# Performance work log

Hardware: AMD Instinct MI355X
Metric: run time of the kernel (lower is better)

## Reference

```python
import jax, jax.numpy as jnp
import numpy as np

N_NODES = 200000   # total graph nodes (var + constraint)
N_VAR   = 112000   # nodes with x[:,0]==1, placed first for static slicing
N_EDGES = 3200000  # avg degree 16
HID     = 64
BATCH   = 64       # fc output width == batch_size in the torch module
TW      = 8        # target_width; TW*(TW-1)=56; N_VAR = seq_len*56 with seq_len=2000


def setup_inputs() -> dict:
    key = jax.random.key(0)
    ks = jax.random.split(key, 8)
    x = jax.random.normal(ks[0], (N_NODES, 2), jnp.float32)
    # var_mask = (x[:,0] == 1): make the first N_VAR nodes variable nodes.
    x = x.at[:, 0].set(jnp.where(jnp.arange(N_NODES) < N_VAR, 1.0, 0.0))
    edge_index = jax.random.randint(ks[1], (2, N_EDGES), 0, N_NODES, jnp.int32)
    W1 = jax.random.normal(ks[2], (2, HID), jnp.float32) / np.sqrt(2.0)
    b1 = jnp.zeros((HID,), jnp.float32)
    W2 = jax.random.normal(ks[3], (HID, HID), jnp.float32) / np.sqrt(HID)
    b2 = jnp.zeros((HID,), jnp.float32)
    Wfc = jax.random.normal(ks[4], (HID, BATCH), jnp.float32) / np.sqrt(HID)
    bfc = jnp.zeros((BATCH,), jnp.float32)
    return {"x": x, "edge_index": edge_index, "W1": W1, "b1": b1,
            "W2": W2, "b2": b2, "Wfc": Wfc, "bfc": bfc}


def gcn_conv(x, src, dst, W, b):
    """PyG GCNConv: transform, then sym-normalized aggregation with self-loops."""
    h = x @ W                                   # [N, F_out]
    ones = jnp.ones(src.shape[0], x.dtype)
    deg = jax.ops.segment_sum(ones, dst, num_segments=N_NODES) + 1.0  # +1: self-loop
    dinv = jax.lax.rsqrt(deg)                   # deg >= 1, always safe
    norm = dinv[src] * dinv[dst]                # [E]
    agg = jax.ops.segment_sum(h[src] * norm[:, None], dst, num_segments=N_NODES)
    agg = agg + h * (dinv * dinv)[:, None]      # self-loop message, norm = dinv_i^2
    return agg + b


def reference(x, edge_index, W1, b1, W2, b2, Wfc, bfc):
    src, dst = edge_index[0], edge_index[1]
    h = jax.nn.relu(gcn_conv(x, src, dst, W1, b1))
    h = gcn_conv(h, src, dst, W2, b2)
    # var_mask == first N_VAR rows by construction (static slice for jit)
    out = jax.nn.relu(h[:N_VAR] @ Wfc + bfc)    # [N_VAR, BATCH]
    width = TW * (TW - 1)                       # 56
    seq_len = N_VAR // width                    # 2000
    return jnp.round(out.reshape(seq_len, BATCH, width))
```

## Files before the change

### kernel.cpp

```cpp
#include <hip/hip_runtime.h>
#include <math.h>

#define N_NODES 200000
#define N_VAR   112000
#define N_EDGES 3200000
#define CAP     64

#define NFINE    512
#define PSZ_F    391
#define FCAP     7168
#define BIN_CHUNK 8192
#define NB_BIN   391
#define NB_L1    12500

typedef int v4i __attribute__((ext_vector_type(4)));

__global__ void __launch_bounds__(512) k_bin(const int* __restrict__ src,
                                             const int* __restrict__ dst,
                                             int* __restrict__ bins,
                                             int* __restrict__ bcnt,
                                             const float* __restrict__ W2,
                                             const float* __restrict__ b2,
                                             const float* __restrict__ Wfc,
                                             const float* __restrict__ bfc,
                                             float* __restrict__ Wc,
                                             float* __restrict__ bc) {
    __shared__ int hist[NFINE];
    __shared__ int seg[NFINE];
    __shared__ int gb[NFINE];
    __shared__ int cur[NFINE];
    __shared__ int wsum[8];
    __shared__ int stg[BIN_CHUNK];
    __shared__ unsigned short stgb[BIN_CHUNK];
    int tid = threadIdx.x;
    int lane = tid & 63, wid = tid >> 6;
    hist[tid] = 0;
    __syncthreads();

    int base = blockIdx.x * BIN_CHUNK;
    int pk[4][4];
    int bk[4][4];
    bool val[4];
    #pragma unroll
    for (int i = 0; i < 4; ++i) {
        int e4 = base + (i * 512 + tid) * 4;
        val[i] = (e4 < N_EDGES);
        if (val[i]) {
            v4i d = __builtin_nontemporal_load((const v4i*)(dst + e4));
            v4i s = __builtin_nontemporal_load((const v4i*)(src + e4));
            int dd[4] = {d.x, d.y, d.z, d.w};
            int ss[4] = {s.x, s.y, s.z, s.w};
            #pragma unroll
            for (int q = 0; q < 4; ++q) {
                int bb2 = dd[q] / PSZ_F;
                int dl = dd[q] - bb2 * PSZ_F;
                pk[i][q] = (dl << 18) | ss[q];
                bk[i][q] = bb2;
                atomicAdd(&hist[bb2], 1);
            }
        }
    }
    __syncthreads();

    int h = hist[tid];
    int inc = h;
    #pragma unroll
    for (int d = 1; d < 64; d <<= 1) {
        int t = __shfl_up(inc, d);
        if (lane >= d) inc += t;
    }
    if (lane == 63) wsum[wid] = inc;
    __syncthreads();
    int pre = 0, tot = 0;
    #pragma unroll
    for (int k = 0; k < 8; ++k) {
        int s = wsum[k];
        pre += (k < wid) ? s : 0;
        tot += s;
    }
    int ex = pre + inc - h;
    seg[tid] = ex;
    cur[tid] = ex;
    gb[tid]  = atomicAdd(&bcnt[tid], h);
    __syncthreads();

    #pragma unroll
    for (int i = 0; i < 4; ++i) {
        if (val[i]) {
            #pragma unroll
            for (int q = 0; q < 4; ++q) {
                int p = atomicAdd(&cur[bk[i][q]], 1);
                stg[p]  = pk[i][q];
                stgb[p] = (unsigned short)bk[i][q];
            }
        }
    }
    __syncthreads();

    for (int i = tid; i < tot; i += 512) {
        int bb2 = stgb[i];
        int pos = gb[bb2] + (i - seg[bb2]);
        if (pos < FCAP)
            bins[(size_t)bb2 * FCAP + pos] = stg[i];
    }

    int b = blockIdx.x;
    if (b < 8) {
        int e = b * 512 + tid;
        int j = e >> 6, l2 = e & 63;
        double acc = 0.0;
        for (int m = 0; m < 64; ++m)
            acc += (double)W2[j * 64 + m] * (double)Wfc[m * 64 + l2];
        Wc[e] = (float)acc;
    } else if (b == 8 && tid < 64) {
        double acc = (double)bfc[tid];
        for (int m = 0; m < 64; ++m)
            acc += (double)b2[m] * (double)Wfc[m * 64 + tid];
        bc[tid] = (float)acc;
    }
}

__global__ void __launch_bounds__(512) k_sort(const int* __restrict__ bins,
                                              const int* __restrict__ bcnt,
                                              const float2* __restrict__ x2,
                                              int* __restrict__ cnt,
                                              float4* __restrict__ xdc,
                                              int* __restrict__ buf) {
    __shared__ int hist[NFINE];
    __shared__ int off[NFINE];
    __shared__ int cur[NFINE];
    __shared__ int wsum[8];
    __shared__ int sorted[FCAP];
    __shared__ unsigned short rowid[FCAP];
    int tid = threadIdx.x;
    int lane = tid & 63, wid = tid >> 6;
    int b = blockIdx.x;
    int n = bcnt[b];
    if (n > FCAP) n = FCAP;
    const int* __restrict__ bp = bins + (size_t)b * FCAP;

    hist[tid] = 0;
    __syncthreads();
    for (int i = tid; i < n; i += 512)
        atomicAdd(&hist[bp[i] >> 18], 1);
    __syncthreads();

    int h = hist[tid];

    int vg = b * PSZ_F + tid;
    if (tid < PSZ_F && vg < N_NODES) {
        cnt[vg] = h;
        float dvv = rsqrtf((float)h + 1.0f);
        float2 xv = x2[vg];
        xdc[vg] = make_float4(xv.x * dvv, xv.y * dvv, dvv, 0.0f);
    }

    int inc = h;
    #pragma unroll
    for (int d = 1; d < 64; d <<= 1) {
        int t = __shfl_up(inc, d);
        if (lane >= d) inc += t;
    }
    if (lane == 63) wsum[wid] = inc;
    __syncthreads();
    int pre = 0;
    #pragma unroll
    for (int k = 0; k < 8; ++k) {
        int s = wsum[k];
        pre += (k < wid) ? s : 0;
    }
    int ex = pre + inc - h;
    off[tid] = ex;
    cur[tid] = ex;
    __syncthreads();

    for (int i = tid; i < n; i += 512) {
        int pkv = bp[i];
        int dl = pkv >> 18;
        int p = atomicAdd(&cur[dl], 1);
        sorted[p] = pkv & 0x3FFFF;
        rowid[p]  = (unsigned short)dl;
    }
    __syncthreads();

    for (int i = tid; i < n; i += 512) {
        int dl = rowid[i];
        int slot = i - off[dl];
        if (slot < CAP)
            buf[(size_t)(b * PSZ_F + dl) * CAP + slot] = sorted[i];
    }
}

__global__ void __launch_bounds__(256, 4) k_l1a(const int* __restrict__ cnt,
                                                const int* __restrict__ buf,
                                                const float4* __restrict__ xdc,
                                                float4* __restrict__ zn) {
    __shared__ __align__(16) float2 pb2[4][64];
    int w = threadIdx.x >> 6, l = threadIdx.x & 63;
    float2* __restrict__ pbw = &pb2[w][0];
    int v0 = blockIdx.x * 16 + w;
    int cc0 = __builtin_amdgcn_readfirstlane(cnt[v0]);
    int cc1 = __builtin_amdgcn_readfirstlane(cnt[v0 + 4]);
    int cc2 = __builtin_amdgcn_readfirstlane(cnt[v0 + 8]);
    int cc3 = __builtin_amdgcn_readfirstlane(cnt[v0 + 12]);

    int nn[4];
    float2 g[4];
    float4 zs[4];
    #pragma unroll
    for (int it = 0; it < 4; ++it) {
        int v = v0 + it * 4;
        int c = (it == 0) ? cc0 : (it == 1) ? cc1 : (it == 2) ? cc2 : cc3;
        int n = (c < CAP) ? c : CAP;
        nn[it] = n;
        int ridx = __builtin_nontemporal_load(buf + v * CAP + l);
        int idx  = (l < n) ? ridx : v;
        g[it]  = *(const float2*)&xdc[idx];
        zs[it] = xdc[v];
    }

    #pragma unroll
    for (int it = 0; it < 4; ++it) {
        int v = v0 + it * 4;
        int n = nn[it];
        float4 self = zs[it];
        float dv = self.z;
        pbw[l] = g[it];

        float ax = self.x, ay = self.y;
        float bx = 0.0f,   by = 0.0f;
        int j = 0;
        for (; j + 16 <= n; j += 16) {
            float4 q0 = *(const float4*)&pbw[j +  0];
            float4 q1 = *(const float4*)&pbw[j +  2];
            float4 q2 = *(const float4*)&pbw[j +  4];
            float4 q3 = *(const float4*)&pbw[j +  6];
            float4 q4 = *(const float4*)&pbw[j +  8];
            float4 q5 = *(const float4*)&pbw[j + 10];
            float4 q6 = *(const float4*)&pbw[j + 12];
            float4 q7 = *(const float4*)&pbw[j + 14];
            ax += q0.x; ay += q0.y;  bx += q0.z; by += q0.w;
            ax += q1.x; ay += q1.y;  bx += q1.z; by += q1.w;
            ax += q2.x; ay += q2.y;  bx += q2.z; by += q2.w;
            ax += q3.x; ay += q3.y;  bx += q3.z; by += q3.w;
            ax += q4.x; ay += q4.y;  bx += q4.z; by += q4.w;
            ax += q5.x; ay += q5.y;  bx += q5.z; by += q5.w;
            ax += q6.x; ay += q6.y;  bx += q6.z; by += q6.w;
            ax += q7.x; ay += q7.y;  bx += q7.z; by += q7.w;
        }
        for (; j + 8 <= n; j += 8) {
            float4 q0 = *(const float4*)&pbw[j + 0];
            float4 q1 = *(const float4*)&pbw[j + 2];
            float4 q2 = *(const float4*)&pbw[j + 4];
            float4 q3 = *(const float4*)&pbw[j + 6];
            ax += q0.x; ay += q0.y;  bx += q0.z; by += q0.w;
            ax += q1.x; ay += q1.y;  bx += q1.z; by += q1.w;
            ax += q2.x; ay += q2.y;  bx += q2.z; by += q2.w;
            ax += q3.x; ay += q3.y;  bx += q3.z; by += q3.w;
        }
        for (; j < n; ++j) {
            float2 q = pbw[j];
            ax += q.x; ay += q.y;
        }
        if (l == 0)
            zn[v] = make_float4((ax + bx) * dv, (ay + by) * dv, dv, 0.0f);
    }
}

__global__ void __launch_bounds__(256, 4) k_l2(const int* __restrict__ cnt,
                                               const int* __restrict__ buf,
                                               const float4* __restrict__ zn,
                                               const float* __restrict__ W1,
                                               const float* __restrict__ b1,
                                               const float* __restrict__ Wc,
                                               const float* __restrict__ bc,
                                               float* __restrict__ out) {
    __shared__ __align__(16) float4 pb[4][64];
    __shared__ __align__(16) float  avs[4][64];
    int w = threadIdx.x >> 6, l = threadIdx.x & 63;
    float4* __restrict__ pbw = &pb[w][0];
    float*  __restrict__ avw = &avs[w][0];
    float wc[64];
    #pragma unroll
    for (int jv = 0; jv < 64; ++jv)
        wc[jv] = Wc[jv * 64 + l];
    float w1a = W1[l], w1b = W1[64 + l], bb = b1[l];
    float bcl = bc[l];
    int v0 = blockIdx.x * 16 + w;
    int cc0 = __builtin_amdgcn_readfirstlane(cnt[v0]);
    int cc1 = __builtin_amdgcn_readfirstlane(cnt[v0 + 4]);
    int cc2 = __builtin_amdgcn_readfirstlane(cnt[v0 + 8]);
    int cc3 = __builtin_amdgcn_readfirstlane(cnt[v0 + 12]);

    int nn[4];
    float4 p[4], zs[4];
    #pragma unroll
    for (int it = 0; it < 4; ++it) {
        int v = v0 + it * 4;
        int c = (it == 0) ? cc0 : (it == 1) ? cc1 : (it == 2) ? cc2 : cc3;
        int n = (c < CAP) ? c : CAP;
        nn[it] = n;
        int ridx = __builtin_nontemporal_load(buf + v * CAP + l);
        int idx  = (l < n) ? ridx : v;
        p[it]  = zn[idx];
        zs[it] = zn[v];
    }

    #pragma unroll
    for (int it = 0; it < 4; ++it) {
        int v = v0 + it * 4;
        int c = (it == 0) ? cc0 : (it == 1) ? cc1 : (it == 2) ? cc2 : cc3;
        int n = nn[it];
        float dv = rsqrtf((float)c + 1.0f);
        float4 zss = zs[it];

        pbw[l] = p[it];

        float acc0 = fmaxf(fmaf(zss.x, w1a, fmaf(zss.y, w1b, bb)), 0.0f) * zss.z;
        float acc1 = 0.0f;
        int j = 0;
        for (; j + 8 <= n; j += 8) {
            float4 q0 = pbw[j+0], q1 = pbw[j+1], q2 = pbw[j+2], q3 = pbw[j+3];
            float4 q4 = pbw[j+4], q5 = pbw[j+5], q6 = pbw[j+6], q7 = pbw[j+7];
            float h0 = fmaxf(fmaf(q0.x, w1a, fmaf(q0.y, w1b, bb)), 0.0f) * q0.z;
            float h1 = fmaxf(fmaf(q1.x, w1a, fmaf(q1.y, w1b, bb)), 0.0f) * q1.z;
            float h2 = fmaxf(fmaf(q2.x, w1a, fmaf(q2.y, w1b, bb)), 0.0f) * q2.z;
            float h3 = fmaxf(fmaf(q3.x, w1a, fmaf(q3.y, w1b, bb)), 0.0f) * q3.z;
            float h4 = fmaxf(fmaf(q4.x, w1a, fmaf(q4.y, w1b, bb)), 0.0f) * q4.z;
            float h5 = fmaxf(fmaf(q5.x, w1a, fmaf(q5.y, w1b, bb)), 0.0f) * q5.z;
            float h6 = fmaxf(fmaf(q6.x, w1a, fmaf(q6.y, w1b, bb)), 0.0f) * q6.z;
            float h7 = fmaxf(fmaf(q7.x, w1a, fmaf(q7.y, w1b, bb)), 0.0f) * q7.z;
            acc0 += (h0 + h1) + (h2 + h3);
            acc1 += (h4 + h5) + (h6 + h7);
        }
        for (; j + 4 <= n; j += 4) {
            float4 q0 = pbw[j+0], q1 = pbw[j+1], q2 = pbw[j+2], q3 = pbw[j+3];
            float h0 = fmaxf(fmaf(q0.x, w1a, fmaf(q0.y, w1b, bb)), 0.0f) * q0.z;
            float h1 = fmaxf(fmaf(q1.x, w1a, fmaf(q1.y, w1b, bb)), 0.0f) * q1.z;
            float h2 = fmaxf(fmaf(q2.x, w1a, fmaf(q2.y, w1b, bb)), 0.0f) * q2.z;
            float h3 = fmaxf(fmaf(q3.x, w1a, fmaf(q3.y, w1b, bb)), 0.0f) * q3.z;
            acc0 += (h0 + h1) + (h2 + h3);
        }
        for (; j < n; ++j) {
            float4 q0 = pbw[j];
            acc1 += fmaxf(fmaf(q0.x, w1a, fmaf(q0.y, w1b, bb)), 0.0f) * q0.z;
        }
        float Av = (acc0 + acc1) * dv;

        avw[l] = Av;

        float t0 = 0.0f, t1 = 0.0f, t2 = 0.0f, t3 = 0.0f;
        #pragma unroll
        for (int jj = 0; jj < 64; jj += 4) {
            float4 a4 = *(const float4*)&avw[jj];
            t0 = fmaf(a4.x, wc[jj + 0], t0);
            t1 = fmaf(a4.y, wc[jj + 1], t1);
            t2 = fmaf(a4.z, wc[jj + 2], t2);
            t3 = fmaf(a4.w, wc[jj + 3], t3);
        }
        float t = ((t0 + t1) + (t2 + t3)) + bcl;
        __builtin_nontemporal_store(rintf(fmaxf(t, 0.0f)), out + v * 64 + l);
    }
}


extern "C" void kernel_launch(void* const* d_in, const int* in_sizes, int n_in,
                              void* d_out, int out_size, void* d_ws, size_t ws_size,
                              hipStream_t stream) {
    const float* x    = (const float*)d_in[0];
    const int*   ei   = (const int*)  d_in[1];
    const float* W1   = (const float*)d_in[2];
    const float* b1   = (const float*)d_in[3];
    const float* W2   = (const float*)d_in[4];
    const float* b2   = (const float*)d_in[5];
    const float* Wfc  = (const float*)d_in[6];
    const float* bfc  = (const float*)d_in[7];
    float* out = (float*)d_out;

    const int* src = ei;
    const int* dst = ei + N_EDGES;

    char* ws = (char*)d_ws;
    int*    cnt    = (int*)   (ws + 0);
    float4* xdc    = (float4*)(ws + 800000);
    int*    bins   = (int*)   (ws + 4000000);
    int*    bcnt   = (int*)   (ws + 18680064);
    float4* zn     = (float4*)(ws + 15204096);
    int*    buf    = (int*)   (ws + 19204096);
    float*  Wc     = (float*) (ws + 70404096);
    float*  bc     = (float*) (ws + 70420480);

    hipMemsetAsync(bcnt, 0, NFINE * sizeof(int), stream);
    k_bin  <<<NB_BIN, 512, 0, stream>>>(src, dst, bins, bcnt, W2, b2, Wfc, bfc, Wc, bc);
    k_sort <<<NFINE, 512, 0, stream>>>(bins, bcnt, (const float2*)x, cnt, xdc, buf);
    k_l1a  <<<NB_L1, 256, 0, stream>>>(cnt, buf, xdc, zn);
    k_l2   <<<N_VAR / 16, 256, 0, stream>>>(cnt, buf, zn, W1, b1, Wc, bc, out);
}
```

Baseline: 198.8 us.

## Switch neighbor lists from padded fixed-cap rows to compact CSR layout

The sort kernel now computes a global exclusive prefix over bin counts and writes neighbor indices contiguously (CSR-style) instead of into 64-slot padded rows per node. The row offset and the degree, clamped to 127, are packed into one int per node. The aggregation kernels decode offset and count and read only valid entries. This shrinks the adjacency buffer and its write and read traffic. The costs are a redundant per-block prefix scan in k_sort and a degree clamp at 127 that could change results for very high-degree nodes.

```diff
diff --git a/kernel.cpp b/kernel.cpp
--- a/kernel.cpp
+++ b/kernel.cpp
@@ -123,37 +123,46 @@
 __global__ void __launch_bounds__(512) k_sort(const int* __restrict__ bins,
                                               const int* __restrict__ bcnt,
                                               const float2* __restrict__ x2,
-                                              int* __restrict__ cnt,
+                                              int* __restrict__ cnt2,
                                               float4* __restrict__ xdc,
-                                              int* __restrict__ buf) {
+                                              int* __restrict__ buf2) {
     __shared__ int hist[NFINE];
     __shared__ int off[NFINE];
     __shared__ int cur[NFINE];
     __shared__ int wsum[8];
-    __shared__ int sorted[FCAP];
-    __shared__ unsigned short rowid[FCAP];
+    __shared__ int ebs;
+    __shared__ int sorted_pk[FCAP];
     int tid = threadIdx.x;
     int lane = tid & 63, wid = tid >> 6;
     int b = blockIdx.x;
-    int n = bcnt[b];
-    if (n > FCAP) n = FCAP;
+
+    int ec = bcnt[tid];
+    if (ec > FCAP) ec = FCAP;
+    int incE = ec;
+    #pragma unroll
+    for (int d = 1; d < 64; d <<= 1) {
+        int t = __shfl_up(incE, d);
+        if (lane >= d) incE += t;
+    }
+    if (lane == 63) wsum[wid] = incE;
+    __syncthreads();
+    int preE = 0;
+    #pragma unroll
+    for (int k = 0; k < 8; ++k)
+        preE += (k < wid) ? wsum[k] : 0;
+    if (tid == b) ebs = preE + incE - ec;
+    hist[tid] = 0;
+    __syncthreads();
+    int ebase = ebs;
+    int nb = bcnt[b];
+    if (nb > FCAP) nb = FCAP;
     const int* __restrict__ bp = bins + (size_t)b * FCAP;
 
-    hist[tid] = 0;
-    __syncthreads();
-    for (int i = tid; i < n; i += 512)
+    for (int i = tid; i < nb; i += 512)
         atomicAdd(&hist[bp[i] >> 18], 1);
     __syncthreads();
 
     int h = hist[tid];
-
-    int vg = b * PSZ_F + tid;
-    if (tid < PSZ_F && vg < N_NODES) {
-        cnt[vg] = h;
-        float dvv = rsqrtf((float)h + 1.0f);
-        float2 xv = x2[vg];
-        xdc[vg] = make_float4(xv.x * dvv, xv.y * dvv, dvv, 0.0f);
-    }
 
     int inc = h;
     #pragma unroll
@@ -165,44 +174,45 @@
     __syncthreads();
     int pre = 0;
     #pragma unroll
-    for (int k = 0; k < 8; ++k) {
-        int s = wsum[k];
-        pre += (k < wid) ? s : 0;
-    }
+    for (int k = 0; k < 8; ++k)
+        pre += (k < wid) ? wsum[k] : 0;
     int ex = pre + inc - h;
     off[tid] = ex;
     cur[tid] = ex;
-    __syncthreads();
-
-    for (int i = tid; i < n; i += 512) {
+
+    int vg = b * PSZ_F + tid;
+    if (tid < PSZ_F && vg < N_NODES) {
+        int ct = (h < 127) ? h : 127;
+        cnt2[vg] = ((ebase + ex) << 7) | ct;
+        float dvv = rsqrtf((float)ct + 1.0f);
+        float2 xv = x2[vg];
+        xdc[vg] = make_float4(xv.x * dvv, xv.y * dvv, dvv, 0.0f);
+    }
+    __syncthreads();
+
+    for (int i = tid; i < nb; i += 512) {
         int pkv = bp[i];
-        int dl = pkv >> 18;
-        int p = atomicAdd(&cur[dl], 1);
-        sorted[p] = pkv & 0x3FFFF;
-        rowid[p]  = (unsigned short)dl;
-    }
-    __syncthreads();
-
-    for (int i = tid; i < n; i += 512) {
-        int dl = rowid[i];
-        int slot = i - off[dl];
-        if (slot < CAP)
-            buf[(size_t)(b * PSZ_F + dl) * CAP + slot] = sorted[i];
-    }
+        int p = atomicAdd(&cur[pkv >> 18], 1);
+        sorted_pk[p] = pkv;
+    }
+    __syncthreads();
+
+    for (int i = tid; i < nb; i += 512)
+        buf2[ebase + i] = sorted_pk[i] & 0x3FFFF;
 }
 
-__global__ void __launch_bounds__(256, 4) k_l1a(const int* __restrict__ cnt,
-                                                const int* __restrict__ buf,
+__global__ void __launch_bounds__(256, 4) k_l1a(const int* __restrict__ cnt2,
+                                                const int* __restrict__ buf2,
                                                 const float4* __restrict__ xdc,
                                                 float4* __restrict__ zn) {
     __shared__ __align__(16) float2 pb2[4][64];
     int w = threadIdx.x >> 6, l = threadIdx.x & 63;
     float2* __restrict__ pbw = &pb2[w][0];
     int v0 = blockIdx.x * 16 + w;
-    int cc0 = __builtin_amdgcn_readfirstlane(cnt[v0]);
-    int cc1 = __builtin_amdgcn_readfirstlane(cnt[v0 + 4]);
-    int cc2 = __builtin_amdgcn_readfirstlane(cnt[v0 + 8]);
-    int cc3 = __builtin_amdgcn_readfirstlane(cnt[v0 + 12]);
+    int q0 = __builtin_amdgcn_readfirstlane(cnt2[v0]);
+    int q1 = __builtin_amdgcn_readfirstlane(cnt2[v0 + 4]);
+    int q2 = __builtin_amdgcn_readfirstlane(cnt2[v0 + 8]);
+    int q3 = __builtin_amdgcn_readfirstlane(cnt2[v0 + 12]);
 
     int nn[4];
     float2 g[4];
@@ -210,12 +220,14 @@
     #pragma unroll
     for (int it = 0; it < 4; ++it) {
         int v = v0 + it * 4;
-        int c = (it == 0) ? cc0 : (it == 1) ? cc1 : (it == 2) ? cc2 : cc3;
+        int q = (it == 0) ? q0 : (it == 1) ? q1 : (it == 2) ? q2 : q3;
+        int c = q & 127;
         int n = (c < CAP) ? c : CAP;
+        int rp = ((unsigned)q) >> 7;
         nn[it] = n;
-        int ridx = __builtin_nontemporal_load(buf + v * CAP + l);
-        int idx  = (l < n) ? ridx : v;
-        g[it]  = *(const float2*)&xdc[idx];
+        int ridx = v;
+        if (l < n) ridx = __builtin_nontemporal_load(buf2 + rp + l);
+        g[it]  = *(const float2*)&xdc[ridx];
         zs[it] = xdc[v];
     }
 
@@ -231,44 +243,44 @@
         float bx = 0.0f,   by = 0.0f;
         int j = 0;
         for (; j + 16 <= n; j += 16) {
-            float4 q0 = *(const float4*)&pbw[j +  0];
-            float4 q1 = *(const float4*)&pbw[j +  2];
-            float4 q2 = *(const float4*)&pbw[j +  4];
-            float4 q3 = *(const float4*)&pbw[j +  6];
-            float4 q4 = *(const float4*)&pbw[j +  8];
-            float4 q5 = *(const float4*)&pbw[j + 10];
-            float4 q6 = *(const float4*)&pbw[j + 12];
-            float4 q7 = *(const float4*)&pbw[j + 14];
-            ax += q0.x; ay += q0.y;  bx += q0.z; by += q0.w;
-            ax += q1.x; ay += q1.y;  bx += q1.z; by += q1.w;
-            ax += q2.x; ay += q2.y;  bx += q2.z; by += q2.w;
-            ax += q3.x; ay += q3.y;  bx += q3.z; by += q3.w;
-            ax += q4.x; ay += q4.y;  bx += q4.z; by += q4.w;
-            ax += q5.x; ay += q5.y;  bx += q5.z; by += q5.w;
-            ax += q6.x; ay += q6.y;  bx += q6.z; by += q6.w;
-            ax += q7.x; ay += q7.y;  bx += q7.z; by += q7.w;
+            float4 t0 = *(const float4*)&pbw[j +  0];
+            float4 t1 = *(const float4*)&pbw[j +  2];
+            float4 t2 = *(const float4*)&pbw[j +  4];
+            float4 t3 = *(const float4*)&pbw[j +  6];
+            float4 t4 = *(const float4*)&pbw[j +  8];
+            float4 t5 = *(const float4*)&pbw[j + 10];
+            float4 t6 = *(const float4*)&pbw[j + 12];
+            float4 t7 = *(const float4*)&pbw[j + 14];
+            ax += t0.x; ay += t0.y;  bx += t0.z; by += t0.w;
+            ax += t1.x; ay += t1.y;  bx += t1.z; by += t1.w;
+            ax += t2.x; ay += t2.y;  bx += t2.z; by += t2.w;
+            ax += t3.x; ay += t3.y;  bx += t3.z; by += t3.w;
+            ax += t4.x; ay += t4.y;  bx += t4.z; by += t4.w;
+            ax += t5.x; ay += t5.y;  bx += t5.z; by += t5.w;
+            ax += t6.x; ay += t6.y;  bx += t6.z; by += t6.w;
+            ax += t7.x; ay += t7.y;  bx += t7.z; by += t7.w;
         }
         for (; j + 8 <= n; j += 8) {
-            float4 q0 = *(const float4*)&pbw[j + 0];
-            float4 q1 = *(const float4*)&pbw[j + 2];
-            float4 q2 = *(const float4*)&pbw[j + 4];
-            float4 q3 = *(const float4*)&pbw[j + 6];
-            ax += q0.x; ay += q0.y;  bx += q0.z; by += q0.w;
-            ax += q1.x; ay += q1.y;  bx += q1.z; by += q1.w;
-            ax += q2.x; ay += q2.y;  bx += q2.z; by += q2.w;
-            ax += q3.x; ay += q3.y;  bx += q3.z; by += q3.w;
+            float4 t0 = *(const float4*)&pbw[j + 0];
+            float4 t1 = *(const float4*)&pbw[j + 2];
+            float4 t2 = *(const float4*)&pbw[j + 4];
+            float4 t3 = *(const float4*)&pbw[j + 6];
+            ax += t0.x; ay += t0.y;  bx += t0.z; by += t0.w;
+            ax += t1.x; ay += t1.y;  bx += t1.z; by += t1.w;
+            ax += t2.x; ay += t2.y;  bx += t2.z; by += t2.w;
+            ax += t3.x; ay += t3.y;  bx += t3.z; by += t3.w;
         }
         for (; j < n; ++j) {
-            float2 q = pbw[j];
-            ax += q.x; ay += q.y;
+            float2 qv = pbw[j];
+            ax += qv.x; ay += qv.y;
         }
         if (l == 0)
             zn[v] = make_float4((ax + bx) * dv, (ay + by) * dv, dv, 0.0f);
     }
 }
 
-__global__ void __launch_bounds__(256, 4) k_l2(const int* __restrict__ cnt,
-                                               const int* __restrict__ buf,
+__global__ void __launch_bounds__(256, 4) k_l2(const int* __restrict__ cnt2,
+                                               const int* __restrict__ buf2,
                                                const float4* __restrict__ zn,
                                                const float* __restrict__ W1,
                                                const float* __restrict__ b1,
@@ -287,31 +299,33 @@
     float w1a = W1[l], w1b = W1[64 + l], bb = b1[l];
     float bcl = bc[l];
     int v0 = blockIdx.x * 16 + w;
-    int cc0 = __builtin_amdgcn_readfirstlane(cnt[v0]);
-    int cc1 = __builtin_amdgcn_readfirstlane(cnt[v0 + 4]);
-    int cc2 = __builtin_amdgcn_readfirstlane(cnt[v0 + 8]);
-    int cc3 = __builtin_amdgcn_readfirstlane(cnt[v0 + 12]);
-
-    int nn[4];
+    int q0 = __builtin_amdgcn_readfirstlane(cnt2[v0]);
+    int q1 = __builtin_amdgcn_readfirstlane(cnt2[v0 + 4]);
+    int q2 = __builtin_amdgcn_readfirstlane(cnt2[v0 + 8]);
+    int q3 = __builtin_amdgcn_readfirstlane(cnt2[v0 + 12]);
+
+    int nn[4], cc[4];
     float4 p[4], zs[4];
     #pragma unroll
     for (int it = 0; it < 4; ++it) {
         int v = v0 + it * 4;
-        int c = (it == 0) ? cc0 : (it == 1) ? cc1 : (it == 2) ? cc2 : cc3;
+        int q = (it == 0) ? q0 : (it == 1) ? q1 : (it == 2) ? q2 : q3;
+        int c = q & 127;
         int n = (c < CAP) ? c : CAP;
+        int rp = ((unsigned)q) >> 7;
         nn[it] = n;
-        int ridx = __builtin_nontemporal_load(buf + v * CAP + l);
-        int idx  = (l < n) ? ridx : v;
-        p[it]  = zn[idx];
+        cc[it] = c;
+        int ridx = v;
+        if (l < n) ridx = __builtin_nontemporal_load(buf2 + rp + l);
+        p[it]  = zn[ridx];
         zs[it] = zn[v];
     }
 
     #pragma unroll
     for (int it = 0; it < 4; ++it) {
         int v = v0 + it * 4;
-        int c = (it == 0) ? cc0 : (it == 1) ? cc1 : (it == 2) ? cc2 : cc3;
         int n = nn[it];
-        float dv = rsqrtf((float)c + 1.0f);
+        float dv = rsqrtf((float)cc[it] + 1.0f);
         float4 zss = zs[it];
 
         pbw[l] = p[it];
@@ -320,30 +334,30 @@
         float acc1 = 0.0f;
         int j = 0;
         for (; j + 8 <= n; j += 8) {
-            float4 q0 = pbw[j+0], q1 = pbw[j+1], q2 = pbw[j+2], q3 = pbw[j+3];
-            float4 q4 = pbw[j+4], q5 = pbw[j+5], q6 = pbw[j+6], q7 = pbw[j+7];
-            float h0 = fmaxf(fmaf(q0.x, w1a, fmaf(q0.y, w1b, bb)), 0.0f) * q0.z;
-            float h1 = fmaxf(fmaf(q1.x, w1a, fmaf(q1.y, w1b, bb)), 0.0f) * q1.z;
-            float h2 = fmaxf(fmaf(q2.x, w1a, fmaf(q2.y, w1b, bb)), 0.0f) * q2.z;
-            float h3 = fmaxf(fmaf(q3.x, w1a, fmaf(q3.y, w1b, bb)), 0.0f) * q3.z;
-            float h4 = fmaxf(fmaf(q4.x, w1a, fmaf(q4.y, w1b, bb)), 0.0f) * q4.z;
-            float h5 = fmaxf(fmaf(q5.x, w1a, fmaf(q5.y, w1b, bb)), 0.0f) * q5.z;
-            float h6 = fmaxf(fmaf(q6.x, w1a, fmaf(q6.y, w1b, bb)), 0.0f) * q6.z;
-            float h7 = fmaxf(fmaf(q7.x, w1a, fmaf(q7.y, w1b, bb)), 0.0f) * q7.z;
+            float4 r0 = pbw[j+0], r1 = pbw[j+1], r2 = pbw[j+2], r3 = pbw[j+3];
+            float4 r4 = pbw[j+4], r5 = pbw[j+5], r6 = pbw[j+6], r7 = pbw[j+7];
+            float h0 = fmaxf(fmaf(r0.x, w1a, fmaf(r0.y, w1b, bb)), 0.0f) * r0.z;
+            float h1 = fmaxf(fmaf(r1.x, w1a, fmaf(r1.y, w1b, bb)), 0.0f) * r1.z;
+            float h2 = fmaxf(fmaf(r2.x, w1a, fmaf(r2.y, w1b, bb)), 0.0f) * r2.z;
+            float h3 = fmaxf(fmaf(r3.x, w1a, fmaf(r3.y, w1b, bb)), 0.0f) * r3.z;
+            float h4 = fmaxf(fmaf(r4.x, w1a, fmaf(r4.y, w1b, bb)), 0.0f) * r4.z;
+            float h5 = fmaxf(fmaf(r5.x, w1a, fmaf(r5.y, w1b, bb)), 0.0f) * r5.z;
+            float h6 = fmaxf(fmaf(r6.x, w1a, fmaf(r6.y, w1b, bb)), 0.0f) * r6.z;
+            float h7 = fmaxf(fmaf(r7.x, w1a, fmaf(r7.y, w1b, bb)), 0.0f) * r7.z;
             acc0 += (h0 + h1) + (h2 + h3);
             acc1 += (h4 + h5) + (h6 + h7);
         }
         for (; j + 4 <= n; j += 4) {
-            float4 q0 = pbw[j+0], q1 = pbw[j+1], q2 = pbw[j+2], q3 = pbw[j+3];
-            float h0 = fmaxf(fmaf(q0.x, w1a, fmaf(q0.y, w1b, bb)), 0.0f) * q0.z;
-            float h1 = fmaxf(fmaf(q1.x, w1a, fmaf(q1.y, w1b, bb)), 0.0f) * q1.z;
-            float h2 = fmaxf(fmaf(q2.x, w1a, fmaf(q2.y, w1b, bb)), 0.0f) * q2.z;
-            float h3 = fmaxf(fmaf(q3.x, w1a, fmaf(q3.y, w1b, bb)), 0.0f) * q3.z;
+            float4 r0 = pbw[j+0], r1 = pbw[j+1], r2 = pbw[j+2], r3 = pbw[j+3];
+            float h0 = fmaxf(fmaf(r0.x, w1a, fmaf(r0.y, w1b, bb)), 0.0f) * r0.z;
+            float h1 = fmaxf(fmaf(r1.x, w1a, fmaf(r1.y, w1b, bb)), 0.0f) * r1.z;
+            float h2 = fmaxf(fmaf(r2.x, w1a, fmaf(r2.y, w1b, bb)), 0.0f) * r2.z;
+            float h3 = fmaxf(fmaf(r3.x, w1a, fmaf(r3.y, w1b, bb)), 0.0f) * r3.z;
             acc0 += (h0 + h1) + (h2 + h3);
         }
         for (; j < n; ++j) {
-            float4 q0 = pbw[j];
-            acc1 += fmaxf(fmaf(q0.x, w1a, fmaf(q0.y, w1b, bb)), 0.0f) * q0.z;
+            float4 r0 = pbw[j];
+            acc1 += fmaxf(fmaf(r0.x, w1a, fmaf(r0.y, w1b, bb)), 0.0f) * r0.z;
         }
         float Av = (acc0 + acc1) * dv;
 
@@ -381,18 +395,18 @@
     const int* dst = ei + N_EDGES;
 
     char* ws = (char*)d_ws;
-    int*    cnt    = (int*)   (ws + 0);
+    int*    cnt2   = (int*)   (ws + 0);
     float4* xdc    = (float4*)(ws + 800000);
     int*    bins   = (int*)   (ws + 4000000);
     int*    bcnt   = (int*)   (ws + 18680064);
     float4* zn     = (float4*)(ws + 15204096);
-    int*    buf    = (int*)   (ws + 19204096);
+    int*    buf2   = (int*)   (ws + 19204096);
     float*  Wc     = (float*) (ws + 70404096);
     float*  bc     = (float*) (ws + 70420480);
 
     hipMemsetAsync(bcnt, 0, NFINE * sizeof(int), stream);
     k_bin  <<<NB_BIN, 512, 0, stream>>>(src, dst, bins, bcnt, W2, b2, Wfc, bfc, Wc, bc);
-    k_sort <<<NFINE, 512, 0, stream>>>(bins, bcnt, (const float2*)x, cnt, xdc, buf);
-    k_l1a  <<<NB_L1, 256, 0, stream>>>(cnt, buf, xdc, zn);
-    k_l2   <<<N_VAR / 16, 256, 0, stream>>>(cnt, buf, zn, W1, b1, Wc, bc, out);
+    k_sort <<<NFINE, 512, 0, stream>>>(bins, bcnt, (const float2*)x, cnt2, xdc, buf2);
+    k_l1a  <<<NB_L1, 256, 0, stream>>>(cnt2, buf2, xdc, zn);
+    k_l2   <<<N_VAR / 16, 256, 0, stream>>>(cnt2, buf2, zn, W1, b1, Wc, bc, out);
 }
```

Result: no change. 201.6 us (+1.4%).
